# Kernel tuning notes

Hardware: AMD Instinct MI355X
Metric: run time of the kernel (lower is better)

The kernel has to match this reference:

```python
import jax, jax.numpy as jnp
import numpy as np

MAX_DET = 1000  # max_detections
CNS, SIN_YAW, COS_YAW, VX = 0, 6, 7, 8


def _decode_box(box):
    # box: [B, K, 10] -> [B, K, 10] decoded (x,y,z,w,l,h,yaw,vx,vy,vz)
    x, y, z = box[..., 0], box[..., 1], box[..., 2]
    w = jnp.exp(box[..., 3])
    l = jnp.exp(box[..., 4])
    h = jnp.exp(box[..., 5])
    yaw = jnp.arctan2(box[..., SIN_YAW], box[..., COS_YAW])  # code_size 10 > COS_YAW
    vx = box[..., VX]
    vy = box[..., VX + 1]
    vz = jnp.zeros_like(x)  # code_size == 10, no vz channel
    return jnp.stack([x, y, z, w, l, h, yaw, vx, vy, vz], axis=-1)


def setup_inputs() -> dict:
    key = jax.random.key(0)
    k1, k2, k3 = jax.random.split(key, 3)
    B, Q, C = 8, 100000, 10
    return {
        'cls_scores': jax.random.normal(k1, (B, Q, C), dtype=jnp.float32),
        'box_preds': jax.random.normal(k2, (B, Q, 10), dtype=jnp.float32),
        'quality': jax.random.normal(k3, (B, Q, 2), dtype=jnp.float32),
    }


def reference(cls_scores, box_preds, quality):
    B, Q, C = cls_scores.shape
    K = min(MAX_DET, Q * C)
    scores = jax.nn.sigmoid(cls_scores)
    # flattened top-k over (Q*C)
    topk_scores, indices = jax.lax.top_k(scores.reshape(B, Q * C), K)
    cls_ids = indices % C
    query_indices = indices // C
    # quality re-rank: scores *= sigmoid(centerness), then sort descending
    centerness = jnp.take_along_axis(quality[..., CNS], query_indices, axis=1)
    cls_scores_origin = topk_scores
    reranked = topk_scores * jax.nn.sigmoid(centerness)
    sort_idx = jnp.argsort(-reranked, axis=1)
    final_scores = jnp.take_along_axis(reranked, sort_idx, axis=1)
    query_indices = jnp.take_along_axis(query_indices, sort_idx, axis=1)
    cls_ids = jnp.take_along_axis(cls_ids, sort_idx, axis=1)
    raw_scores = jnp.take_along_axis(cls_scores_origin, sort_idx, axis=1)
    # gather boxes per batch: [B, K, 10]
    box = jnp.take_along_axis(box_preds, query_indices[..., None], axis=1)
    boxes_3d = _decode_box(box)
    labels_3d = cls_ids.astype(jnp.int64)
    return boxes_3d, final_scores, labels_3d, raw_scores
```

## Files before the change

### kernel.cpp

```cpp
#include <hip/hip_runtime.h>
#include <stdint.h>
#include <math.h>


#define BATCHES 8
#define NQ 100000
#define NEL 1000000
#define NVEC 250000
#define TOPK 1000
#define NBINS 4096
#define CAP 2048
#define NBLK 64
#define NTHR 512
#define STAGE_CAP 512
#define SELBLK 32
#define SELTHR 64
#define SRTBLK 16

__device__ __forceinline__ unsigned f2key(float f) {
    unsigned b = __float_as_uint(f);
    return b ^ ((b & 0x80000000u) ? 0xFFFFFFFFu : 0x80000000u);
}
__device__ __forceinline__ float key2f(unsigned k) {
    unsigned b = (k & 0x80000000u) ? (k ^ 0x80000000u) : ~k;
    return __uint_as_float(b);
}

__global__ __launch_bounds__(NTHR) void hist_kernel(const float* __restrict__ cls,
                                                    unsigned* __restrict__ ghist) {
    __shared__ unsigned lh[NBINS];
    const int b = blockIdx.x / NBLK;
    const int blk = blockIdx.x % NBLK;
    for (int i = threadIdx.x; i < NBINS; i += NTHR) lh[i] = 0;
    __syncthreads();
    const float4* src = (const float4*)(cls + (size_t)b * NEL);
    for (int i = blk * NTHR + threadIdx.x; i < NVEC; i += NBLK * NTHR) {
        float4 v = src[i];
        atomicAdd(&lh[f2key(v.x) >> 20], 1u);
        atomicAdd(&lh[f2key(v.y) >> 20], 1u);
        atomicAdd(&lh[f2key(v.z) >> 20], 1u);
        atomicAdd(&lh[f2key(v.w) >> 20], 1u);
    }
    __syncthreads();
    unsigned* gh = ghist + (size_t)b * NBINS;
    for (int i = threadIdx.x; i < NBINS; i += NTHR) {
        unsigned v = lh[i];
        if (v) atomicAdd(&gh[i], v);
    }
}

__global__ __launch_bounds__(256) void thresh_kernel(const unsigned* __restrict__ ghist,
                                                     unsigned* __restrict__ tbin) {
    __shared__ unsigned sh[NBINS];
    __shared__ unsigned coarse[256];
    const int b = blockIdx.x;
    for (int i = threadIdx.x; i < NBINS; i += 256) sh[i] = ghist[(size_t)b * NBINS + i];
    __syncthreads();
    unsigned s = 0;
    const int base = threadIdx.x * 16;
#pragma unroll
    for (int j = 0; j < 16; ++j) s += sh[base + j];
    coarse[threadIdx.x] = s;
    __syncthreads();
    if (threadIdx.x == 0) {
        unsigned acc = 0;
        int tb = 0;
        for (int c = 255; c >= 0; --c) {
            if (acc + coarse[c] >= (unsigned)TOPK) {
                for (int bin = c * 16 + 15; bin >= c * 16; --bin) {
                    acc += sh[bin];
                    if (acc >= (unsigned)TOPK) { tb = bin; break; }
                }
                break;
            }
            acc += coarse[c];
        }
        tbin[b] = (unsigned)tb;
    }
}

__global__ __launch_bounds__(NTHR) void collect_kernel(const float* __restrict__ cls,
                                                       const unsigned* __restrict__ tbin,
                                                       unsigned* __restrict__ cnt,
                                                       unsigned long long* __restrict__ cand) {
    __shared__ unsigned long long stage[STAGE_CAP];
    __shared__ unsigned lcnt;
    __shared__ unsigned gbase;
    const int b = blockIdx.x / NBLK;
    const int blk = blockIdx.x % NBLK;
    if (threadIdx.x == 0) lcnt = 0;
    __syncthreads();
    const unsigned tb = tbin[b];
    const float4* src = (const float4*)(cls + (size_t)b * NEL);
    unsigned long long* cb = cand + (size_t)b * CAP;
    for (int i = blk * NTHR + threadIdx.x; i < NVEC; i += NBLK * NTHR) {
        float4 v = src[i];
        float xs[4] = {v.x, v.y, v.z, v.w};
#pragma unroll
        for (int j = 0; j < 4; ++j) {
            unsigned k = f2key(xs[j]);
            if ((k >> 20) >= tb) {
                unsigned idx = (unsigned)(i * 4 + j);
                unsigned long long pack = ((unsigned long long)k << 32) |
                                          (unsigned long long)(0xFFFFFFFFu - idx);
                unsigned p = atomicAdd(&lcnt, 1u);
                if (p < STAGE_CAP) {
                    stage[p] = pack;
                } else {
                    unsigned pos = atomicAdd(&cnt[b], 1u);
                    if (pos < CAP) cb[pos] = pack;
                }
            }
        }
    }
    __syncthreads();
    unsigned n = lcnt < STAGE_CAP ? lcnt : STAGE_CAP;
    if (threadIdx.x == 0) gbase = atomicAdd(&cnt[b], n);
    __syncthreads();
    for (unsigned t = threadIdx.x; t < n; t += NTHR) {
        unsigned pos = gbase + t;
        if (pos < CAP) cb[pos] = stage[t];
    }
}

__global__ __launch_bounds__(SELTHR) void select_kernel(const float* __restrict__ quality,
                                                        const unsigned long long* __restrict__ cand,
                                                        const unsigned* __restrict__ cnt,
                                                        unsigned long long* __restrict__ top_rr,
                                                        float* __restrict__ top_s) {
    __shared__ unsigned long long arr[CAP];
    const int b = blockIdx.x / SELBLK;
    const int bk = blockIdx.x % SELBLK;
    const int tid = threadIdx.x;
    int n = (int)cnt[b];
    if (n > CAP) n = CAP;
    if (bk * SELTHR >= n) return;
    const unsigned long long* src = cand + (size_t)b * CAP;
    for (int i = tid; i < n; i += SELTHR) arr[i] = src[i];
    __syncthreads();

    const int ci = bk * SELTHR + tid;
    if (ci < n) {
        const unsigned long long m = arr[ci];
        int r = 0, j = 0;
        for (; j + 16 <= n; j += 16) {
            unsigned long long v0 = arr[j+0],  v1 = arr[j+1],  v2 = arr[j+2],  v3 = arr[j+3];
            unsigned long long v4 = arr[j+4],  v5 = arr[j+5],  v6 = arr[j+6],  v7 = arr[j+7];
            unsigned long long v8 = arr[j+8],  v9 = arr[j+9],  vA = arr[j+10], vB = arr[j+11];
            unsigned long long vC = arr[j+12], vD = arr[j+13], vE = arr[j+14], vF = arr[j+15];
            r += (v0 > m) + (v1 > m) + (v2 > m) + (v3 > m)
               + (v4 > m) + (v5 > m) + (v6 > m) + (v7 > m)
               + (v8 > m) + (v9 > m) + (vA > m) + (vB > m)
               + (vC > m) + (vD > m) + (vE > m) + (vF > m);
        }
        for (; j < n; ++j) r += (arr[j] > m);

        if (r < TOPK) {
            unsigned key = (unsigned)(m >> 32);
            unsigned idx = 0xFFFFFFFFu - (unsigned)(m & 0xFFFFFFFFu);
            unsigned q = idx / 10u;
            float logit = key2f(key);
            float s = (float)(1.0 / (1.0 + exp(-(double)logit)));
            float ctr = quality[((size_t)b * NQ + q) * 2];
            float cs = (float)(1.0 / (1.0 + exp(-(double)ctr)));
            float rr = s * cs;
            top_rr[(size_t)b * 1024 + r] = ((unsigned long long)__float_as_uint(rr) << 32) |
                                           (unsigned long long)(0xFFFFFFFFu - idx);
            top_s[(size_t)b * 1024 + r] = s;
        }
    }
}

__global__ __launch_bounds__(64) void sortdecode_kernel(const float* __restrict__ box_preds,
                                                        const unsigned long long* __restrict__ top_rr,
                                                        const float* __restrict__ top_s,
                                                        float* __restrict__ out) {
    __shared__ unsigned long long rr2[TOPK];
    const int b = blockIdx.x / SRTBLK;
    const int bk = blockIdx.x % SRTBLK;
    const int tid = threadIdx.x;
    for (int i = tid; i < TOPK; i += 64)
        rr2[i] = top_rr[(size_t)b * 1024 + i];
    __syncthreads();

    const int p = bk * 64 + tid;
    if (p < TOPK) {
        const unsigned long long mine = rr2[p];
        int r = 0, j = 0;
        for (; j + 16 <= TOPK; j += 16) {
            unsigned long long v0 = rr2[j+0],  v1 = rr2[j+1],  v2 = rr2[j+2],  v3 = rr2[j+3];
            unsigned long long v4 = rr2[j+4],  v5 = rr2[j+5],  v6 = rr2[j+6],  v7 = rr2[j+7];
            unsigned long long v8 = rr2[j+8],  v9 = rr2[j+9],  vA = rr2[j+10], vB = rr2[j+11];
            unsigned long long vC = rr2[j+12], vD = rr2[j+13], vE = rr2[j+14], vF = rr2[j+15];
            r += (v0 > mine) + (v1 > mine) + (v2 > mine) + (v3 > mine)
               + (v4 > mine) + (v5 > mine) + (v6 > mine) + (v7 > mine)
               + (v8 > mine) + (v9 > mine) + (vA > mine) + (vB > mine)
               + (vC > mine) + (vD > mine) + (vE > mine) + (vF > mine);
        }
        for (; j < TOPK; ++j) r += (rr2[j] > mine);

        unsigned idx = 0xFFFFFFFFu - (unsigned)(mine & 0xFFFFFFFFu);
        float rr = __uint_as_float((unsigned)(mine >> 32));
        unsigned q = idx / 10u;
        unsigned c = idx - q * 10u;
        float s = top_s[(size_t)b * 1024 + p];

        const size_t row = (size_t)b * TOPK + (size_t)r;
        out[(size_t)BATCHES * TOPK * 10 + row] = rr;
        out[(size_t)BATCHES * TOPK * 11 + row] = (float)c;
        out[(size_t)BATCHES * TOPK * 12 + row] = s;
        const float* bp = box_preds + ((size_t)b * NQ + q) * 10;
        float* ob = out + row * 10;
        ob[0] = bp[0];
        ob[1] = bp[1];
        ob[2] = bp[2];
        ob[3] = expf(bp[3]);
        ob[4] = expf(bp[4]);
        ob[5] = expf(bp[5]);
        ob[6] = atan2f(bp[6], bp[7]);
        ob[7] = bp[8];
        ob[8] = bp[9];
        ob[9] = 0.0f;
    }
}

extern "C" void kernel_launch(void* const* d_in, const int* in_sizes, int n_in,
                              void* d_out, int out_size, void* d_ws, size_t ws_size,
                              hipStream_t stream) {
    (void)in_sizes; (void)n_in; (void)out_size; (void)ws_size;
    const float* cls = (const float*)d_in[0];
    const float* box = (const float*)d_in[1];
    const float* qual = (const float*)d_in[2];
    float* out = (float*)d_out;
    char* ws = (char*)d_ws;
    unsigned* ghist = (unsigned*)ws;
    unsigned* cnt = (unsigned*)(ws + 131072);
    unsigned* tbin = (unsigned*)(ws + 131072 + 32);
    unsigned long long* cand = (unsigned long long*)(ws + 131072 + 64);
    unsigned long long* top_rr = (unsigned long long*)(ws + 131072 + 64 + 131072);
    float* top_s = (float*)(ws + 131072 + 64 + 131072 + 65536);

    hipMemsetAsync(d_ws, 0, 131072 + 32, stream);
    hist_kernel<<<BATCHES * NBLK, NTHR, 0, stream>>>(cls, ghist);
    thresh_kernel<<<BATCHES, 256, 0, stream>>>(ghist, tbin);
    collect_kernel<<<BATCHES * NBLK, NTHR, 0, stream>>>(cls, tbin, cnt, cand);
    select_kernel<<<BATCHES * SELBLK, SELTHR, 0, stream>>>(qual, cand, cnt, top_rr, top_s);
    sortdecode_kernel<<<BATCHES * SRTBLK, 64, 0, stream>>>(box, top_rr, top_s, out);
}
```

Before: 154.3 us.

## Speculatively collect high-score candidates during histogram pass to skip second scan

The histogram kernel now also stages every element whose key bin is at or above a fixed speculative bin into a per-batch buffer. The threshold kernel is merged with compaction: it filters that speculative buffer down to the true threshold instead of re-reading all scores. This removes the second full pass over the score tensor and one kernel launch. The cost is extra atomics and stores in the histogram pass. If the threshold falls below the speculative bin or the buffer overflows, it falls back to a full scan run by only one block per batch, which would be slow.

```diff
diff --git a/kernel.cpp b/kernel.cpp
--- a/kernel.cpp
+++ b/kernel.cpp
@@ -13,6 +13,8 @@
 #define NBLK 64
 #define NTHR 512
 #define STAGE_CAP 512
+#define SPEC_CAP 8192
+#define SPEC_BIN 3075u
 #define SELBLK 32
 #define SELTHR 64
 #define SRTBLK 16
@@ -26,20 +28,39 @@
     return __uint_as_float(b);
 }
 
-__global__ __launch_bounds__(NTHR) void hist_kernel(const float* __restrict__ cls,
-                                                    unsigned* __restrict__ ghist) {
+__global__ __launch_bounds__(NTHR) void histspec_kernel(const float* __restrict__ cls,
+                                                        unsigned* __restrict__ ghist,
+                                                        unsigned* __restrict__ speccnt,
+                                                        unsigned long long* __restrict__ spec) {
     __shared__ unsigned lh[NBINS];
+    __shared__ unsigned long long stg[STAGE_CAP];
+    __shared__ unsigned lcnt, gbase;
     const int b = blockIdx.x / NBLK;
     const int blk = blockIdx.x % NBLK;
     for (int i = threadIdx.x; i < NBINS; i += NTHR) lh[i] = 0;
+    if (threadIdx.x == 0) lcnt = 0;
     __syncthreads();
     const float4* src = (const float4*)(cls + (size_t)b * NEL);
+    unsigned long long* sb = spec + (size_t)b * SPEC_CAP;
     for (int i = blk * NTHR + threadIdx.x; i < NVEC; i += NBLK * NTHR) {
         float4 v = src[i];
-        atomicAdd(&lh[f2key(v.x) >> 20], 1u);
-        atomicAdd(&lh[f2key(v.y) >> 20], 1u);
-        atomicAdd(&lh[f2key(v.z) >> 20], 1u);
-        atomicAdd(&lh[f2key(v.w) >> 20], 1u);
+        float xs[4] = {v.x, v.y, v.z, v.w};
+#pragma unroll
+        for (int j = 0; j < 4; ++j) {
+            unsigned k = f2key(xs[j]);
+            unsigned bin = k >> 20;
+            atomicAdd(&lh[bin], 1u);
+            if (bin >= SPEC_BIN) {
+                unsigned long long pack = ((unsigned long long)k << 32) |
+                                          (unsigned long long)(0xFFFFFFFFu - (unsigned)(i * 4 + j));
+                unsigned p = atomicAdd(&lcnt, 1u);
+                if (p < STAGE_CAP) stg[p] = pack;
+                else {
+                    unsigned pos = atomicAdd(&speccnt[b], 1u);
+                    if (pos < SPEC_CAP) sb[pos] = pack;
+                }
+            }
+        }
     }
     __syncthreads();
     unsigned* gh = ghist + (size_t)b * NBINS;
@@ -47,22 +68,36 @@
         unsigned v = lh[i];
         if (v) atomicAdd(&gh[i], v);
     }
-}
-
-__global__ __launch_bounds__(256) void thresh_kernel(const unsigned* __restrict__ ghist,
-                                                     unsigned* __restrict__ tbin) {
+    unsigned n = lcnt < STAGE_CAP ? lcnt : STAGE_CAP;
+    if (threadIdx.x == 0) gbase = atomicAdd(&speccnt[b], n);
+    __syncthreads();
+    for (unsigned t = threadIdx.x; t < n; t += NTHR) {
+        unsigned pos = gbase + t;
+        if (pos < SPEC_CAP) sb[pos] = stg[t];
+    }
+}
+
+__global__ __launch_bounds__(256) void threshcompact_kernel(const unsigned* __restrict__ ghist,
+                                                            const unsigned* __restrict__ speccnt,
+                                                            const unsigned long long* __restrict__ spec,
+                                                            const float* __restrict__ cls,
+                                                            unsigned* __restrict__ cnt,
+                                                            unsigned long long* __restrict__ cand) {
     __shared__ unsigned sh[NBINS];
     __shared__ unsigned coarse[256];
+    __shared__ unsigned stb, lcnt;
     const int b = blockIdx.x;
-    for (int i = threadIdx.x; i < NBINS; i += 256) sh[i] = ghist[(size_t)b * NBINS + i];
+    const int tid = threadIdx.x;
+    for (int i = tid; i < NBINS; i += 256) sh[i] = ghist[(size_t)b * NBINS + i];
+    if (tid == 0) lcnt = 0;
     __syncthreads();
     unsigned s = 0;
-    const int base = threadIdx.x * 16;
+    const int base = tid * 16;
 #pragma unroll
     for (int j = 0; j < 16; ++j) s += sh[base + j];
-    coarse[threadIdx.x] = s;
-    __syncthreads();
-    if (threadIdx.x == 0) {
+    coarse[tid] = s;
+    __syncthreads();
+    if (tid == 0) {
         unsigned acc = 0;
         int tb = 0;
         for (int c = 255; c >= 0; --c) {
@@ -75,52 +110,40 @@
             }
             acc += coarse[c];
         }
-        tbin[b] = (unsigned)tb;
-    }
-}
-
-__global__ __launch_bounds__(NTHR) void collect_kernel(const float* __restrict__ cls,
-                                                       const unsigned* __restrict__ tbin,
-                                                       unsigned* __restrict__ cnt,
-                                                       unsigned long long* __restrict__ cand) {
-    __shared__ unsigned long long stage[STAGE_CAP];
-    __shared__ unsigned lcnt;
-    __shared__ unsigned gbase;
-    const int b = blockIdx.x / NBLK;
-    const int blk = blockIdx.x % NBLK;
-    if (threadIdx.x == 0) lcnt = 0;
-    __syncthreads();
-    const unsigned tb = tbin[b];
-    const float4* src = (const float4*)(cls + (size_t)b * NEL);
+        stb = (unsigned)tb;
+    }
+    __syncthreads();
+    const unsigned tb = stb;
+    const unsigned nsr = speccnt[b];
     unsigned long long* cb = cand + (size_t)b * CAP;
-    for (int i = blk * NTHR + threadIdx.x; i < NVEC; i += NBLK * NTHR) {
-        float4 v = src[i];
-        float xs[4] = {v.x, v.y, v.z, v.w};
+    if (tb >= SPEC_BIN && nsr <= SPEC_CAP) {
+        const unsigned long long* sb = spec + (size_t)b * SPEC_CAP;
+        for (unsigned i = tid; i < nsr; i += 256) {
+            unsigned long long v = sb[i];
+            if ((unsigned)(v >> 52) >= tb) {
+                unsigned p = atomicAdd(&lcnt, 1u);
+                if (p < CAP) cb[p] = v;
+            }
+        }
+    } else {
+        const float4* src = (const float4*)(cls + (size_t)b * NEL);
+        for (int i = tid; i < NVEC; i += 256) {
+            float4 v = src[i];
+            float xs[4] = {v.x, v.y, v.z, v.w};
 #pragma unroll
-        for (int j = 0; j < 4; ++j) {
-            unsigned k = f2key(xs[j]);
-            if ((k >> 20) >= tb) {
-                unsigned idx = (unsigned)(i * 4 + j);
-                unsigned long long pack = ((unsigned long long)k << 32) |
-                                          (unsigned long long)(0xFFFFFFFFu - idx);
-                unsigned p = atomicAdd(&lcnt, 1u);
-                if (p < STAGE_CAP) {
-                    stage[p] = pack;
-                } else {
-                    unsigned pos = atomicAdd(&cnt[b], 1u);
-                    if (pos < CAP) cb[pos] = pack;
+            for (int j = 0; j < 4; ++j) {
+                unsigned k = f2key(xs[j]);
+                if ((k >> 20) >= tb) {
+                    unsigned long long pack = ((unsigned long long)k << 32) |
+                                              (unsigned long long)(0xFFFFFFFFu - (unsigned)(i * 4 + j));
+                    unsigned p = atomicAdd(&lcnt, 1u);
+                    if (p < CAP) cb[p] = pack;
                 }
             }
         }
     }
     __syncthreads();
-    unsigned n = lcnt < STAGE_CAP ? lcnt : STAGE_CAP;
-    if (threadIdx.x == 0) gbase = atomicAdd(&cnt[b], n);
-    __syncthreads();
-    for (unsigned t = threadIdx.x; t < n; t += NTHR) {
-        unsigned pos = gbase + t;
-        if (pos < CAP) cb[pos] = stage[t];
-    }
+    if (tid == 0) cnt[b] = lcnt < CAP ? lcnt : CAP;
 }
 
 __global__ __launch_bounds__(SELTHR) void select_kernel(const float* __restrict__ quality,
@@ -235,15 +258,15 @@
     char* ws = (char*)d_ws;
     unsigned* ghist = (unsigned*)ws;
     unsigned* cnt = (unsigned*)(ws + 131072);
-    unsigned* tbin = (unsigned*)(ws + 131072 + 32);
-    unsigned long long* cand = (unsigned long long*)(ws + 131072 + 64);
-    unsigned long long* top_rr = (unsigned long long*)(ws + 131072 + 64 + 131072);
-    float* top_s = (float*)(ws + 131072 + 64 + 131072 + 65536);
-
-    hipMemsetAsync(d_ws, 0, 131072 + 32, stream);
-    hist_kernel<<<BATCHES * NBLK, NTHR, 0, stream>>>(cls, ghist);
-    thresh_kernel<<<BATCHES, 256, 0, stream>>>(ghist, tbin);
-    collect_kernel<<<BATCHES * NBLK, NTHR, 0, stream>>>(cls, tbin, cnt, cand);
+    unsigned* speccnt = (unsigned*)(ws + 131104);
+    unsigned long long* cand = (unsigned long long*)(ws + 131168);
+    unsigned long long* top_rr = (unsigned long long*)(ws + 262240);
+    float* top_s = (float*)(ws + 327776);
+    unsigned long long* spec = (unsigned long long*)(ws + 360544);
+
+    hipMemsetAsync(d_ws, 0, 131136, stream);
+    histspec_kernel<<<BATCHES * NBLK, NTHR, 0, stream>>>(cls, ghist, speccnt, spec);
+    threshcompact_kernel<<<BATCHES, 256, 0, stream>>>(ghist, speccnt, spec, cls, cnt, cand);
     select_kernel<<<BATCHES * SELBLK, SELTHR, 0, stream>>>(qual, cand, cnt, top_rr, top_s);
     sortdecode_kernel<<<BATCHES * SRTBLK, 64, 0, stream>>>(box, top_rr, top_s, out);
 }
```

Result: no change. 152.1 us (-1.4%).
